# Kernel optimization log

Hardware: AMD Instinct MI355X
Metric: run time of the kernel (lower is better)

## Reference

```python
import jax, jax.numpy as jnp
import numpy as np

G = 56          # voxel grid resolution per axis
N = 65536
K = 27          # 3x3x3 kernel offsets
C_IN = 128
C_OUT = 128


def _build_rulebook():
    """Submanifold conv rulebook: for each kernel offset, (input_row, output_row) pairs.

    Padded to P=N pairs per offset; invalid pairs use in_idx=0 and out_idx=N
    (a dummy output slot that is dropped), so shapes are static.
    """
    rng = np.random.default_rng(0)
    keys = np.sort(rng.choice(G ** 3, size=N, replace=False)).astype(np.int64)
    x = keys // (G * G)
    y = (keys // G) % G
    z = keys % G
    in_idx = np.zeros((K, N), dtype=np.int32)
    out_idx = np.full((K, N), N, dtype=np.int32)
    k = 0
    for dx in (-1, 0, 1):
        for dy in (-1, 0, 1):
            for dz in (-1, 0, 1):
                nx, ny, nz = x + dx, y + dy, z + dz
                valid = (nx >= 0) & (nx < G) & (ny >= 0) & (ny < G) & (nz >= 0) & (nz < G)
                nkey = (nx * G + ny) * G + nz
                pos = np.searchsorted(keys, np.clip(nkey, 0, G ** 3 - 1))
                pos = np.clip(pos, 0, N - 1)
                found = valid & (keys[pos] == nkey)
                cnt = int(found.sum())
                in_idx[k, :cnt] = pos[found]
                out_idx[k, :cnt] = np.nonzero(found)[0]
                k += 1
    return jnp.asarray(in_idx), jnp.asarray(out_idx)


def setup_inputs() -> dict:
    key = jax.random.key(0)
    k1, k2, k3 = jax.random.split(key, 3)
    fan_in = K * C_IN
    features = jax.random.normal(k1, (N, C_IN), dtype=jnp.float32)
    weight = jax.random.normal(k2, (K, C_IN, C_OUT), dtype=jnp.float32) * (1.0 / np.sqrt(fan_in))
    bias = jax.random.normal(k3, (C_OUT,), dtype=jnp.float32) * 0.01
    in_idx, out_idx = _build_rulebook()
    return {"features": features, "weight": weight, "bias": bias,
            "in_idx": in_idx, "out_idx": out_idx}


def reference(features, weight, bias, in_idx, out_idx):
    # gather: [K, P, C_in]
    gathered = features[in_idx]
    # per-offset GEMM: [K, P, C_out]
    contrib = jnp.einsum('kpc,kcd->kpd', gathered, weight)
    n = features.shape[0]
    c_out = weight.shape[-1]
    # scatter-accumulate into N real rows + 1 dummy row for padded pairs
    out = jnp.zeros((n + 1, c_out), dtype=features.dtype)
    out = out.at[out_idx.reshape(-1)].add(contrib.reshape(-1, c_out))
    return out[:n] + bias
```

## Files before the change

kernel.cpp:

```cpp
#include <hip/hip_runtime.h>
#include <hip/hip_bf16.h>
#include <stdint.h>

#define NV   65536
#define KOFF 27
#define CIN  128
#define COUT 128
#define NSEC (NV + 128)

typedef __bf16 bf16x8 __attribute__((ext_vector_type(8)));
typedef float  f32x4  __attribute__((ext_vector_type(4)));

__device__ __forceinline__ void async_copy16(void* lds, const void* g) {
    __builtin_amdgcn_global_load_lds(
        (const __attribute__((address_space(1))) void*)g,
        (__attribute__((address_space(3))) void*)lds,
        16, 0, 0);
}

#define JOB_A_BLOCKS 4097
#define JOB_B_BLOCKS 216
#define JOB_S_BLOCKS 1728

__global__ void k_prep_all(const float* __restrict__ f,
                           uint4* __restrict__ fb4,
                           const float* __restrict__ w,
                           uint4* __restrict__ wfrag4,
                           const int4* __restrict__ in4,
                           const int4* __restrict__ out4,
                           int* __restrict__ nbr) {
    const int b = blockIdx.x;
    const int t = threadIdx.x;
    if (b < JOB_A_BLOCKS) {
        int i = b * 256 + t;
        int total8  = (NV + 1) * CIN / 8;
        int nvalid8 = NV * CIN / 8;
        if (i >= total8) return;
        union { uint4 u; __hip_bfloat16 h[8]; } p;
        if (i < nvalid8) {
            const float4* f4 = (const float4*)f;
            float4 a = f4[i * 2];
            float4 c = f4[i * 2 + 1];
            p.h[0] = __float2bfloat16(a.x);
            p.h[1] = __float2bfloat16(a.y);
            p.h[2] = __float2bfloat16(a.z);
            p.h[3] = __float2bfloat16(a.w);
            p.h[4] = __float2bfloat16(c.x);
            p.h[5] = __float2bfloat16(c.y);
            p.h[6] = __float2bfloat16(c.z);
            p.h[7] = __float2bfloat16(c.w);
        } else {
            p.u = make_uint4(0, 0, 0, 0);
        }
        fb4[i] = p.u;
    } else if (b < JOB_A_BLOCKS + JOB_B_BLOCKS) {
        int c    = (b - JOB_A_BLOCKS) * 256 + t;
        int lane = c & 63;
        int nt   = (c >> 6) & 1;
        int ks   = (c >> 7) & 3;
        int wv   = (c >> 9) & 3;
        int k    = c >> 11;
        int cout = wv * 32 + nt * 16 + (lane & 15);
        int cin0 = ks * 32 + (lane >> 4) * 8;
        const float* wk = w + k * 16384;
        union { uint4 u; __hip_bfloat16 h[8]; } p;
        #pragma unroll
        for (int j = 0; j < 8; ++j)
            p.h[j] = __float2bfloat16(wk[(cin0 + j) * 128 + cout]);
        wfrag4[c] = p.u;
    } else {
        int i = (b - JOB_A_BLOCKS - JOB_B_BLOCKS) * 256 + t;
        int k = i >> 14;
        int4 ii = in4[i];
        int4 oo = out4[i];
        int* nb = nbr + (size_t)k * NSEC;
        auto POS = [](int o) {
            return (o >> 7) * 128 + (o & 15) * 8 + ((o >> 4) & 7);
        };
        nb[POS(oo.x)] = ii.x;
        nb[POS(oo.y)] = ii.y;
        nb[POS(oo.z)] = ii.z;
        nb[POS(oo.w)] = ii.w;
    }
}

__global__ __launch_bounds__(256, 2)
void sp_conv_main(const __hip_bfloat16* __restrict__ feats,
                  const uint4* __restrict__ wfrag,
                  const int* __restrict__ nbrt,
                  const float* __restrict__ bias,
                  float* __restrict__ out) {
    __shared__ unsigned char smem[65536];

    const int t   = threadIdx.x;
    const int bid = blockIdx.x;
    const int tile0 = ((bid & 7) * 64 + (bid >> 3)) * 128;

    const int w    = t >> 6;
    const int lane = t & 63;
    const int lr   = lane & 15;
    const int quad = lane >> 4;

    const int srow  = t >> 4;
    const int sbyte = ((t & 15) ^ srow) * 16;

    f32x4 acc[8][2] = {};

    const unsigned char* featsB = (const unsigned char*)feats;

    int  arows[8];
    uint4 bA[4][2], bB[4][2];

    auto NLOAD = [&](int k) {
        const int4* np = (const int4*)(nbrt + (size_t)k * NSEC + tile0 + srow * 8);
        int4 a0 = np[0];
        int4 a1 = np[1];
        arows[0] = a0.x; arows[1] = a0.y; arows[2] = a0.z; arows[3] = a0.w;
        arows[4] = a1.x; arows[5] = a1.y; arows[6] = a1.z; arows[7] = a1.w;
    };
    auto STAGE = [&](int sb) {
        #pragma unroll
        for (int i = 0; i < 8; ++i) {
            unsigned ar = min((unsigned)arows[i], (unsigned)NV);
            async_copy16(smem + sb + i * 4096 + t * 16,
                         featsB + (size_t)ar * 256 + sbyte);
        }
    };
    auto BLOAD = [&](const uint4* wfk, uint4 (&b)[4][2]) {
        #pragma unroll
        for (int ks = 0; ks < 4; ++ks)
            #pragma unroll
            for (int nt = 0; nt < 2; ++nt)
                b[ks][nt] = wfk[ks * 128 + nt * 64];
    };
    auto AFLOAD = [&](int rb, int ks, bf16x8 (&af)[8]) {
        #pragma unroll
        for (int mt = 0; mt < 8; ++mt)
            af[mt] = *(const bf16x8*)(smem + rb + (mt * 16 + lr) * 256 +
                                      (((ks * 4 + quad) ^ lr) * 16));
    };
    auto MFMA16 = [&](bf16x8 (&af)[8], uint4 (&b)[2]) {
        #pragma unroll
        for (int mt = 0; mt < 8; ++mt)
            #pragma unroll
            for (int nt = 0; nt < 2; ++nt)
                acc[mt][nt] = __builtin_amdgcn_mfma_f32_16x16x32_bf16(
                    af[mt], *(const bf16x8*)&b[nt], acc[mt][nt], 0, 0, 0);
    };

    NLOAD(0);
    STAGE(0);
    __builtin_amdgcn_sched_barrier(0);
    NLOAD(1);
    BLOAD(wfrag + w * 512 + lane, bA);
    asm volatile("s_waitcnt vmcnt(10)" ::: "memory");
    __builtin_amdgcn_s_barrier();
    __builtin_amdgcn_sched_barrier(0);

    auto ITER = [&](int k, int rb, uint4 (&buse)[4][2], uint4 (&bload)[4][2]) {
        STAGE(rb ^ 32768);
        __builtin_amdgcn_sched_barrier(0);
        NLOAD(min(k + 2, KOFF - 1));
        BLOAD(wfrag + (k + 1) * 2048 + w * 512 + lane, bload);
        #pragma unroll
        for (int ks = 0; ks < 4; ++ks) {
            bf16x8 af[8];
            AFLOAD(rb, ks, af);
            __builtin_amdgcn_s_setprio(1);
            MFMA16(af, buse[ks]);
            __builtin_amdgcn_s_setprio(0);
        }
        __builtin_amdgcn_sched_barrier(0);
        asm volatile("s_waitcnt vmcnt(10)" ::: "memory");
        __builtin_amdgcn_s_barrier();
        __builtin_amdgcn_sched_barrier(0);
    };

    #pragma unroll 1
    for (int kk = 0; kk < KOFF - 1; kk += 2) {
        ITER(kk,     0,     bA, bB);
        ITER(kk + 1, 32768, bB, bA);
    }

    #pragma unroll
    for (int ks = 0; ks < 4; ++ks) {
        bf16x8 af[8];
        AFLOAD(0, ks, af);
        MFMA16(af, bA[ks]);
    }

    const int n0w = w * 32;
    float bv[2];
    #pragma unroll
    for (int nt = 0; nt < 2; ++nt) bv[nt] = bias[n0w + nt * 16 + lr];

    #pragma unroll
    for (int mt = 0; mt < 8; ++mt) {
        #pragma unroll
        for (int nt = 0; nt < 2; ++nt) {
            #pragma unroll
            for (int r = 0; r < 4; ++r) {
                int grow = tile0 + mt * 16 + quad * 4 + r;
                out[(size_t)grow * COUT + n0w + nt * 16 + lr] =
                    acc[mt][nt][r] + bv[nt];
            }
        }
    }
}


extern "C" void kernel_launch(void* const* d_in, const int* in_sizes, int n_in,
                              void* d_out, int out_size, void* d_ws, size_t ws_size,
                              hipStream_t stream) {
    const float* features = (const float*)d_in[0];
    const float* weight   = (const float*)d_in[1];
    const float* bias     = (const float*)d_in[2];
    const int*   in_idx   = (const int*)d_in[3];
    const int*   out_idx  = (const int*)d_in[4];
    float* out = (float*)d_out;

    uint8_t* ws = (uint8_t*)d_ws;
    size_t off = 0;
    __hip_bfloat16* feats_bf = (__hip_bfloat16*)(ws + off);
    off += (size_t)(NV + 1) * CIN * 2;
    off = (off + 255) & ~(size_t)255;
    uint4* wfrag = (uint4*)(ws + off);
    off += (size_t)KOFF * CIN * COUT * 2;
    off = (off + 255) & ~(size_t)255;
    int* nbr = (int*)(ws + off);

    hipMemsetAsync(nbr, 0xFF, (size_t)KOFF * NSEC * 4, stream);

    k_prep_all<<<JOB_A_BLOCKS + JOB_B_BLOCKS + JOB_S_BLOCKS, 256, 0, stream>>>(
        features, (uint4*)feats_bf, weight, wfrag,
        (const int4*)in_idx, (const int4*)out_idx, nbr);

    sp_conv_main<<<NV / 128, 256, 0, stream>>>(feats_bf, wfrag, nbr, bias, out);
}
```

Before: 151.6 us.

## Process two 128-row output tiles per block to reuse weight fragments

```diff
diff --git a/kernel.cpp b/kernel.cpp
--- a/kernel.cpp
+++ b/kernel.cpp
@@ -94,7 +94,9 @@
 
     const int t   = threadIdx.x;
     const int bid = blockIdx.x;
-    const int tile0 = ((bid & 7) * 64 + (bid >> 3)) * 128;
+    const int p    = (bid & 7) * 32 + (bid >> 3);
+    const int t0A  = (p * 2) * 128;
+    const int t0B  = (p * 2 + 1) * 128;
 
     const int w    = t >> 6;
     const int lane = t & 63;
@@ -104,15 +106,15 @@
     const int srow  = t >> 4;
     const int sbyte = ((t & 15) ^ srow) * 16;
 
-    f32x4 acc[8][2] = {};
+    f32x4 acc0[8][2] = {};
+    f32x4 acc1[8][2] = {};
+    uint4 bA[4][2], bB[4][2];
+    int arows[8];
 
     const unsigned char* featsB = (const unsigned char*)feats;
 
-    int  arows[8];
-    uint4 bA[4][2], bB[4][2];
-
-    auto NLOAD = [&](int k) {
-        const int4* np = (const int4*)(nbrt + (size_t)k * NSEC + tile0 + srow * 8);
+    auto NLOAD = [&](int k, int tbase) {
+        const int4* np = (const int4*)(nbrt + (size_t)k * NSEC + tbase + srow * 8);
         int4 a0 = np[0];
         int4 a1 = np[1];
         arows[0] = a0.x; arows[1] = a0.y; arows[2] = a0.z; arows[3] = a0.w;
@@ -133,61 +135,69 @@
             for (int nt = 0; nt < 2; ++nt)
                 b[ks][nt] = wfk[ks * 128 + nt * 64];
     };
-    auto AFLOAD = [&](int rb, int ks, bf16x8 (&af)[8]) {
-        #pragma unroll
-        for (int mt = 0; mt < 8; ++mt)
-            af[mt] = *(const bf16x8*)(smem + rb + (mt * 16 + lr) * 256 +
-                                      (((ks * 4 + quad) ^ lr) * 16));
-    };
-    auto MFMA16 = [&](bf16x8 (&af)[8], uint4 (&b)[2]) {
-        #pragma unroll
-        for (int mt = 0; mt < 8; ++mt)
-            #pragma unroll
-            for (int nt = 0; nt < 2; ++nt)
-                acc[mt][nt] = __builtin_amdgcn_mfma_f32_16x16x32_bf16(
-                    af[mt], *(const bf16x8*)&b[nt], acc[mt][nt], 0, 0, 0);
-    };
-
-    NLOAD(0);
+    auto COMPUTE = [&](int rb, uint4 (&buse)[4][2], f32x4 (&ac)[8][2]) {
+        #pragma unroll
+        for (int ks = 0; ks < 4; ++ks) {
+            bf16x8 af[8];
+            #pragma unroll
+            for (int mt = 0; mt < 8; ++mt)
+                af[mt] = *(const bf16x8*)(smem + rb + (mt * 16 + lr) * 256 +
+                                          (((ks * 4 + quad) ^ lr) * 16));
+            #pragma unroll
+            for (int mt = 0; mt < 8; ++mt)
+                #pragma unroll
+                for (int nt = 0; nt < 2; ++nt)
+                    ac[mt][nt] = __builtin_amdgcn_mfma_f32_16x16x32_bf16(
+                        af[mt], *(const bf16x8*)&buse[ks][nt],
+                        ac[mt][nt], 0, 0, 0);
+        }
+    };
+
+    auto PHA = [&](int k, uint4 (&buse)[4][2]) {
+        STAGE(32768);
+        __builtin_amdgcn_sched_barrier(0);
+        NLOAD(min(k + 1, KOFF - 1), t0A);
+        COMPUTE(0, buse, acc0);
+        __builtin_amdgcn_sched_barrier(0);
+        asm volatile("s_waitcnt vmcnt(2)" ::: "memory");
+        __builtin_amdgcn_s_barrier();
+        __builtin_amdgcn_sched_barrier(0);
+    };
+    auto PHB = [&](int k, uint4 (&buse)[4][2], uint4 (&bload)[4][2]) {
+        STAGE(0);
+        __builtin_amdgcn_sched_barrier(0);
+        NLOAD(min(k + 1, KOFF - 1), t0B);
+        BLOAD(wfrag + (k + 1) * 2048 + w * 512 + lane, bload);
+        COMPUTE(32768, buse, acc1);
+        __builtin_amdgcn_sched_barrier(0);
+        asm volatile("s_waitcnt vmcnt(10)" ::: "memory");
+        __builtin_amdgcn_s_barrier();
+        __builtin_amdgcn_sched_barrier(0);
+    };
+
+    NLOAD(0, t0A);
     STAGE(0);
     __builtin_amdgcn_sched_barrier(0);
-    NLOAD(1);
+    NLOAD(0, t0B);
     BLOAD(wfrag + w * 512 + lane, bA);
     asm volatile("s_waitcnt vmcnt(10)" ::: "memory");
     __builtin_amdgcn_s_barrier();
     __builtin_amdgcn_sched_barrier(0);
 
-    auto ITER = [&](int k, int rb, uint4 (&buse)[4][2], uint4 (&bload)[4][2]) {
-        STAGE(rb ^ 32768);
-        __builtin_amdgcn_sched_barrier(0);
-        NLOAD(min(k + 2, KOFF - 1));
-        BLOAD(wfrag + (k + 1) * 2048 + w * 512 + lane, bload);
-        #pragma unroll
-        for (int ks = 0; ks < 4; ++ks) {
-            bf16x8 af[8];
-            AFLOAD(rb, ks, af);
-            __builtin_amdgcn_s_setprio(1);
-            MFMA16(af, buse[ks]);
-            __builtin_amdgcn_s_setprio(0);
-        }
-        __builtin_amdgcn_sched_barrier(0);
-        asm volatile("s_waitcnt vmcnt(10)" ::: "memory");
-        __builtin_amdgcn_s_barrier();
-        __builtin_amdgcn_sched_barrier(0);
-    };
-
     #pragma unroll 1
     for (int kk = 0; kk < KOFF - 1; kk += 2) {
-        ITER(kk,     0,     bA, bB);
-        ITER(kk + 1, 32768, bB, bA);
+        PHA(kk,     bA);
+        PHB(kk,     bA, bB);
+        PHA(kk + 1, bB);
+        PHB(kk + 1, bB, bA);
     }
 
-    #pragma unroll
-    for (int ks = 0; ks < 4; ++ks) {
-        bf16x8 af[8];
-        AFLOAD(0, ks, af);
-        MFMA16(af, bA[ks]);
-    }
+    STAGE(32768);
+    __builtin_amdgcn_sched_barrier(0);
+    COMPUTE(0, bA, acc0);
+    asm volatile("s_waitcnt vmcnt(0)" ::: "memory");
+    __builtin_amdgcn_s_barrier();
+    COMPUTE(32768, bA, acc1);
 
     const int n0w = w * 32;
     float bv[2];
@@ -200,9 +210,10 @@
         for (int nt = 0; nt < 2; ++nt) {
             #pragma unroll
             for (int r = 0; r < 4; ++r) {
-                int grow = tile0 + mt * 16 + quad * 4 + r;
-                out[(size_t)grow * COUT + n0w + nt * 16 + lr] =
-                    acc[mt][nt][r] + bv[nt];
+                int rr = mt * 16 + quad * 4 + r;
+                int cc = n0w + nt * 16 + lr;
+                out[(size_t)(t0A + rr) * COUT + cc] = acc0[mt][nt][r] + bv[nt];
+                out[(size_t)(t0B + rr) * COUT + cc] = acc1[mt][nt][r] + bv[nt];
             }
         }
     }
@@ -235,5 +246,5 @@
         features, (uint4*)feats_bf, weight, wfrag,
         (const int4*)in_idx, (const int4*)out_idx, nbr);
 
-    sp_conv_main<<<NV / 128, 256, 0, stream>>>(feats_bf, wfrag, nbr, bias, out);
-}
+    sp_conv_main<<<256, 256, 0, stream>>>(feats_bf, wfrag, nbr, bias, out);
+}
```

Result: slower. 172.6 us (+13.9%).
